# Performance work log

Measured on AMD Instinct MI355X. Metric: run time of the kernel, lower is better.

The kernel has to match this reference:

```python
import jax, jax.numpy as jnp
import numpy as np

N_NODES = 100000
N_EDGES = 800000


def gcn_layer(x, W, b, src, dst, n):
    # PyG GCNConv (normalize=True): x @ W, add self-loops, sym-normalized mean aggregation, + bias
    h = x @ W  # [N, out]
    deg = jax.ops.segment_sum(jnp.ones_like(src, dtype=h.dtype), dst, num_segments=n)
    dinv = jnp.where(deg > 0, jax.lax.rsqrt(jnp.maximum(deg, 1.0)), 0.0)
    norm = dinv[src] * dinv[dst]  # [E+N]
    msg = h[src] * norm[:, None]  # gather + scale
    out = jax.ops.segment_sum(msg, dst, num_segments=n)  # scatter-add
    return out + b


def setup_inputs() -> dict:
    key = jax.random.key(0)
    k1, k2, k3, k4 = jax.random.split(key, 4)
    x = jax.random.normal(k1, (N_NODES, 128), dtype=jnp.float32)
    edge_index = jax.random.randint(k2, (2, N_EDGES), 0, N_NODES, dtype=jnp.int64)
    W1 = jax.random.normal(k3, (128, 64), dtype=jnp.float32) * (1.0 / np.sqrt(128))
    b1 = jnp.zeros((64,), dtype=jnp.float32)
    W2 = jax.random.normal(k4, (64, 40), dtype=jnp.float32) * (1.0 / np.sqrt(64))
    b2 = jnp.zeros((40,), dtype=jnp.float32)
    return {"x": x, "edge_index": edge_index, "W1": W1, "b1": b1, "W2": W2, "b2": b2}


def reference(x, edge_index, W1, b1, W2, b2):
    n = x.shape[0]
    loop = jnp.arange(n, dtype=edge_index.dtype)
    src = jnp.concatenate([edge_index[0], loop])  # add self-loops
    dst = jnp.concatenate([edge_index[1], loop])
    h = jax.nn.relu(gcn_layer(x, W1, b1, src, dst, n))
    # dropout is identity in eval mode (self.training=False)
    out = gcn_layer(h, W2, b2, src, dst, n)
    return jax.nn.log_softmax(out, axis=1)
```

## Files before the change

kernel.cpp:

```cpp
#include <hip/hip_runtime.h>
#include <hip/hip_fp16.h>
#include <math.h>


typedef _Float16 f16x4 __attribute__((ext_vector_type(4)));
typedef _Float16 f16x8 __attribute__((ext_vector_type(8)));
typedef float    f32x4 __attribute__((ext_vector_type(4)));

__global__ void zero_kernel(int* __restrict__ p, int n) {
    int i = blockIdx.x * blockDim.x + threadIdx.x;
    if (i < n) p[i] = 0;
}

__global__ void deg_rank_kernel(const int* __restrict__ dst, int* __restrict__ degi,
                                int* __restrict__ rank, int E) {
    int i = blockIdx.x * blockDim.x + threadIdx.x;
    if (i < E) rank[i] = atomicAdd(&degi[dst[i]], 1);
}

__global__ __launch_bounds__(256) void blocksum_kernel(const int* __restrict__ degi,
                                                       int* __restrict__ partial, int n) {
    __shared__ int sm[256];
    int t = threadIdx.x;
    int base = blockIdx.x * 1024 + t * 4;
    int s = 0;
#pragma unroll
    for (int j = 0; j < 4; ++j) { int i = base + j; if (i < n) s += degi[i]; }
    sm[t] = s;
    __syncthreads();
    for (int off = 128; off > 0; off >>= 1) {
        if (t < off) sm[t] += sm[t + off];
        __syncthreads();
    }
    if (t == 0) partial[blockIdx.x] = sm[0];
}

__global__ __launch_bounds__(256) void offsets_kernel(int* __restrict__ degi,
                                                      const int* __restrict__ partial,
                                                      int* __restrict__ rowstart,
                                                      int n, int nb) {
    __shared__ int sm[256];
    __shared__ int pbase_s;
    int t = threadIdx.x;
    int pv = (t < nb) ? partial[t] : 0;
    sm[t] = pv;
    __syncthreads();
    for (int off = 1; off < 256; off <<= 1) {
        int x = (t >= off) ? sm[t - off] : 0;
        __syncthreads();
        sm[t] += x;
        __syncthreads();
    }
    if (t == 0) pbase_s = (blockIdx.x > 0) ? sm[blockIdx.x - 1] : 0;
    __syncthreads();
    int pbase = pbase_s;
    __syncthreads();

    int base = blockIdx.x * 1024 + t * 4;
    int v[4]; int s = 0;
#pragma unroll
    for (int j = 0; j < 4; ++j) { v[j] = (base + j < n) ? degi[base + j] : 0; s += v[j]; }
    sm[t] = s;
    __syncthreads();
    for (int off = 1; off < 256; off <<= 1) {
        int x = (t >= off) ? sm[t - off] : 0;
        __syncthreads();
        sm[t] += x;
        __syncthreads();
    }
    int run = pbase + (sm[t] - s);
#pragma unroll
    for (int j = 0; j < 4; ++j) {
        if (base + j < n) {
            rowstart[base + j] = run; run += v[j];
            ((float*)degi)[base + j] = rsqrtf((float)v[j] + 1.0f);
        }
    }
}

__global__ void fill_kernel(const int* __restrict__ src, const int* __restrict__ dst,
                            const int* __restrict__ rank, const float* __restrict__ dinv,
                            const int* __restrict__ rowstart, int2* __restrict__ csr, int E) {
    int e = blockIdx.x * blockDim.x + threadIdx.x;
    if (e >= E) return;
    int s = src[e], t = dst[e];
    float nrm = dinv[s] * dinv[t];
    unsigned short us = __half_as_ushort(__float2half_rn(nrm));
    int packed = (int)(((unsigned)us << 16) | us);
    int pos = rowstart[t] + rank[e];
    csr[pos] = make_int2(s, packed);
}

__global__ __launch_bounds__(256) void gemm1_mfma(const float* __restrict__ X,
                                                  const float* __restrict__ W,
                                                  _Float16* __restrict__ H, int n) {
    __shared__ _Float16 Xs[64 * 128];
    __shared__ _Float16 Ws[64 * 128];
    int t = threadIdx.x;
    int rowbase = blockIdx.x * 64;

    for (int i = t; i < 2048; i += 256) {
        int row = i >> 5;
        int k = (i & 31) * 4;
        int gr = rowbase + row; if (gr >= n) gr = n - 1;
        float4 v = *reinterpret_cast<const float4*>(X + (size_t)gr * 128 + k);
        f16x4 hv = { (_Float16)v.x, (_Float16)v.y, (_Float16)v.z, (_Float16)v.w };
        int idx = row * 128 + (k ^ ((row & 7) << 3));
        *reinterpret_cast<f16x4*>(&Xs[idx]) = hv;
    }
    for (int i = t; i < 2048; i += 256) {
        int k = i >> 4;
        int nn0 = (i & 15) * 4;
        float4 v = *reinterpret_cast<const float4*>(W + (size_t)k * 64 + nn0);
        const float* vp = reinterpret_cast<const float*>(&v);
#pragma unroll
        for (int j = 0; j < 4; ++j) {
            int nn = nn0 + j;
            Ws[nn * 128 + (k ^ ((nn & 7) << 3))] = (_Float16)vp[j];
        }
    }
    __syncthreads();

    int w = t >> 6;
    int l = t & 63;
    int lr = l & 15;
    int lk = l >> 4;
    int arow = 16 * w + lr;

    f16x8 a[4];
#pragma unroll
    for (int kc = 0; kc < 4; ++kc) {
        int k8 = kc * 32 + lk * 8;
        a[kc] = *reinterpret_cast<f16x8*>(&Xs[arow * 128 + (k8 ^ ((arow & 7) << 3))]);
    }
    f32x4 acc[4] = {};
#pragma unroll
    for (int nt = 0; nt < 4; ++nt) {
        int nrow = 16 * nt + lr;
#pragma unroll
        for (int kc = 0; kc < 4; ++kc) {
            int k8 = kc * 32 + lk * 8;
            f16x8 b = *reinterpret_cast<f16x8*>(&Ws[nrow * 128 + (k8 ^ ((nrow & 7) << 3))]);
            acc[nt] = __builtin_amdgcn_mfma_f32_16x16x32_f16(a[kc], b, acc[nt], 0, 0, 0);
        }
    }
#pragma unroll
    for (int nt = 0; nt < 4; ++nt) {
#pragma unroll
        for (int r = 0; r < 4; ++r) {
            int grow = rowbase + 16 * w + lk * 4 + r;
            if (grow < n) H[(size_t)grow * 64 + nt * 16 + lr] = (_Float16)acc[nt][r];
        }
    }
}

static __device__ __forceinline__ __half2 relu_h2(__half2 v) {
    unsigned u = *reinterpret_cast<unsigned*>(&v);
    unsigned neg = (u >> 15) & 0x00010001u;
    u &= ~(neg * 0xFFFFu);
    return *reinterpret_cast<__half2*>(&u);
}

template <bool RELU, bool BIAS>
__global__ __launch_bounds__(256) void gather64h_kernel(const __half* __restrict__ Hh,
                                                        const int2* __restrict__ csr,
                                                        const int* __restrict__ rowstart,
                                                        const float* __restrict__ dinv,
                                                        const float* __restrict__ b,
                                                        __half* __restrict__ Oh, int n, int E) {
    int gt = blockIdx.x * blockDim.x + threadIdx.x;
    int node = gt >> 3;
    if (node >= n) return;
    int fl = gt & 7;
    const float4* H4 = reinterpret_cast<const float4*>(Hh);
    int rs = rowstart[node];
    int re = (node + 1 < n) ? rowstart[node + 1] : E;
    __half2 acc[4];
#pragma unroll
    for (int q = 0; q < 4; ++q) acc[q] = __float2half2_rn(0.0f);

    int e = rs;
    while (__any(e < re)) {
        int srcrow[4]; __half2 nh[4]; float4 raw[4];
#pragma unroll
        for (int u = 0; u < 4; ++u) {
            int ee = e + u;
            bool valid = ee < re;
            int2 c = csr[valid ? ee : rs];
            srcrow[u] = valid ? c.x : 0;
            int ni = valid ? c.y : 0;
            nh[u] = *reinterpret_cast<__half2*>(&ni);
        }
#pragma unroll
        for (int u = 0; u < 4; ++u)
            raw[u] = H4[srcrow[u] * 8 + fl];
#pragma unroll
        for (int u = 0; u < 4; ++u) {
            const __half2* hp = reinterpret_cast<const __half2*>(&raw[u]);
#pragma unroll
            for (int q = 0; q < 4; ++q)
                acc[q] = __hfma2(hp[q], nh[u], acc[q]);
        }
        e += 4;
    }
    {
        float di = dinv[node];
        __half2 d2 = __float2half2_rn(di * di);
        float4 raw = H4[node * 8 + fl];
        const __half2* hp = reinterpret_cast<const __half2*>(&raw);
#pragma unroll
        for (int q = 0; q < 4; ++q) acc[q] = __hfma2(hp[q], d2, acc[q]);
    }
    if (BIAS) {
        float4 b0 = reinterpret_cast<const float4*>(b)[fl * 2];
        float4 b1 = reinterpret_cast<const float4*>(b)[fl * 2 + 1];
        acc[0] = __hadd2(acc[0], __float22half2_rn(make_float2(b0.x, b0.y)));
        acc[1] = __hadd2(acc[1], __float22half2_rn(make_float2(b0.z, b0.w)));
        acc[2] = __hadd2(acc[2], __float22half2_rn(make_float2(b1.x, b1.y)));
        acc[3] = __hadd2(acc[3], __float22half2_rn(make_float2(b1.z, b1.w)));
    }
    if (RELU) {
#pragma unroll
        for (int q = 0; q < 4; ++q) acc[q] = relu_h2(acc[q]);
    }
    float4 o;
    __half2* op = reinterpret_cast<__half2*>(&o);
#pragma unroll
    for (int q = 0; q < 4; ++q) op[q] = acc[q];
    *reinterpret_cast<float4*>(Oh + (size_t)node * 64 + fl * 8) = o;
}

__global__ __launch_bounds__(256) void gemm2_softmax_kernel(const __half* __restrict__ Xh,
                                                            const float* __restrict__ W,
                                                            const float* __restrict__ b,
                                                            float* __restrict__ out, int n) {
    constexpr int BM = 96, K = 64, C = 40, XP = 68, HP = 41;
    __shared__ float Xs[BM * XP];
    __shared__ float Ws[K * C];
    __shared__ float bs[C];
    __shared__ float rowm[BM], rowls[BM];
    int t = threadIdx.x;
    int tx = t % (C / 4);
    int ty = t / (C / 4);
    bool active = ty < BM / 4;
    int rowbase = blockIdx.x * BM;

    for (int i = t; i < K * C / 4; i += 256)
        ((float4*)Ws)[i] = ((const float4*)W)[i];
    if (t < C) bs[t] = b[t];
    for (int fi = t; fi < BM * 8; fi += 256) {
        int row = fi >> 3, kq = fi & 7;
        int gr = rowbase + row; if (gr >= n) gr = n - 1;
        float4 raw = reinterpret_cast<const float4*>(Xh + (size_t)gr * K)[kq];
        const __half2* hp = reinterpret_cast<const __half2*>(&raw);
        float2 f0 = __half22float2(hp[0]), f1 = __half22float2(hp[1]);
        float2 f2 = __half22float2(hp[2]), f3 = __half22float2(hp[3]);
        float* dp = &Xs[row * XP + kq * 8];
        *reinterpret_cast<float4*>(dp)     = make_float4(f0.x, f0.y, f1.x, f1.y);
        *reinterpret_cast<float4*>(dp + 4) = make_float4(f2.x, f2.y, f3.x, f3.y);
    }
    __syncthreads();

    float acc[4][4] = {};
    if (active) {
#pragma unroll
        for (int k0 = 0; k0 < K; k0 += 4) {
            float4 xq[4], wq[4];
#pragma unroll
            for (int i = 0; i < 4; ++i)
                xq[i] = *reinterpret_cast<const float4*>(&Xs[(ty * 4 + i) * XP + k0]);
#pragma unroll
            for (int j = 0; j < 4; ++j)
                wq[j] = *reinterpret_cast<const float4*>(&Ws[(k0 + j) * C + tx * 4]);
#pragma unroll
            for (int i = 0; i < 4; ++i) {
                const float* xa = reinterpret_cast<const float*>(&xq[i]);
#pragma unroll
                for (int j = 0; j < 4; ++j) {
                    const float* wb = reinterpret_cast<const float*>(&wq[j]);
                    acc[i][0] += xa[j] * wb[0];
                    acc[i][1] += xa[j] * wb[1];
                    acc[i][2] += xa[j] * wb[2];
                    acc[i][3] += xa[j] * wb[3];
                }
            }
        }
    }
    __syncthreads();
    float* Hs = Xs;
    if (active) {
#pragma unroll
        for (int i = 0; i < 4; ++i) {
            int r = ty * 4 + i;
#pragma unroll
            for (int j = 0; j < 4; ++j)
                Hs[r * HP + tx * 4 + j] = acc[i][j] + bs[tx * 4 + j];
        }
    }
    __syncthreads();
    if (t < BM) {
        float m = -INFINITY;
        for (int j = 0; j < C; ++j) m = fmaxf(m, Hs[t * HP + j]);
        float s = 0.f;
        for (int j = 0; j < C; ++j) s += __expf(Hs[t * HP + j] - m);
        rowm[t] = m; rowls[t] = __logf(s);
    }
    __syncthreads();
    for (int idx = t; idx < BM * C; idx += 256) {
        int r = idx / C, c = idx - r * C;
        int gr = rowbase + r;
        if (gr < n) out[(size_t)gr * C + c] = Hs[r * HP + c] - rowm[r] - rowls[r];
    }
}

extern "C" void kernel_launch(void* const* d_in, const int* in_sizes, int n_in,
                              void* d_out, int out_size, void* d_ws, size_t ws_size,
                              hipStream_t stream) {
    const float* x  = (const float*)d_in[0];
    const int*   ei = (const int*)d_in[1];
    const float* W1 = (const float*)d_in[2];
    const float* b1 = (const float*)d_in[3];
    const float* W2 = (const float*)d_in[4];
    const float* b2 = (const float*)d_in[5];
    float* out = (float*)d_out;

    const int n = in_sizes[0] / 128;
    const int E = in_sizes[1] / 2;
    const int* src = ei;
    const int* dst = ei + E;

    auto al = [](size_t x) { return (x + 255) & ~(size_t)255; };
    float* ws = (float*)d_ws;
    size_t o_deg  = 0;
    size_t o_cnt  = al(n);
    size_t o_part = o_cnt + al(n);
    size_t o_rank = o_part + 1024;
    size_t o_csr  = o_rank + al(E);
    size_t o_h1   = o_csr + al((size_t)2 * E);
    size_t o_out1 = o_h1 + al((size_t)n * 32);

    int*    degi     = (int*)(ws + o_deg);
    float*  dinv     = (float*)(ws + o_deg);
    int*    rowstart = (int*)(ws + o_cnt);
    int*    partial  = (int*)(ws + o_part);
    int*    rank     = (int*)(ws + o_rank);
    int2*   csr      = (int2*)(ws + o_csr);
    __half* h1       = (__half*)(ws + o_h1);
    __half* out1     = (__half*)(ws + o_out1);
    __half* agg2     = (__half*)(ws + o_h1);

    const int NB = (n + 1023) / 1024;

    zero_kernel<<<(n + 255) / 256, 256, 0, stream>>>(degi, n);
    deg_rank_kernel<<<(E + 255) / 256, 256, 0, stream>>>(dst, degi, rank, E);
    blocksum_kernel<<<NB, 256, 0, stream>>>(degi, partial, n);
    offsets_kernel<<<NB, 256, 0, stream>>>(degi, partial, rowstart, n, NB);
    fill_kernel<<<(E + 255) / 256, 256, 0, stream>>>(src, dst, rank, dinv, rowstart, csr, E);

    gemm1_mfma<<<(n + 63) / 64, 256, 0, stream>>>(x, W1, (_Float16*)h1, n);
    gather64h_kernel<true, true><<<((size_t)n * 8 + 255) / 256, 256, 0, stream>>>(
        h1, csr, rowstart, dinv, b1, out1, n, E);
    gather64h_kernel<false, false><<<((size_t)n * 8 + 255) / 256, 256, 0, stream>>>(
        out1, csr, rowstart, dinv, nullptr, agg2, n, E);
    gemm2_softmax_kernel<<<(n + 95) / 96, 256, 0, stream>>>(agg2, W2, b2, out, n);
}
```

Baseline: 144.2 us.

## Fuse layer-2 gather into GEMM2+softmax and load X directly into MFMA registers

The second-layer neighbor aggregation now runs inside the GEMM2/log-softmax kernel. Each block gathers 64 rows into shared memory and then applies W2 and the softmax, so the fp16 agg2 intermediate is never written to or read back from global memory, and one launch is removed. GEMM1 also stops staging X through LDS: each lane loads its fp32 A fragment straight from global memory and converts it to fp16 in registers. The cost is a smaller row tile per block (64 instead of 96), so W2 is reloaded by more blocks, and the gather's irregular latency now sits in front of the GEMM inside one block.

```diff
diff --git a/kernel.cpp b/kernel.cpp
--- a/kernel.cpp
+++ b/kernel.cpp
@@ -3,7 +3,6 @@
 #include <math.h>
 
 
-typedef _Float16 f16x4 __attribute__((ext_vector_type(4)));
 typedef _Float16 f16x8 __attribute__((ext_vector_type(8)));
 typedef float    f32x4 __attribute__((ext_vector_type(4)));
 
@@ -94,20 +93,10 @@
 __global__ __launch_bounds__(256) void gemm1_mfma(const float* __restrict__ X,
                                                   const float* __restrict__ W,
                                                   _Float16* __restrict__ H, int n) {
-    __shared__ _Float16 Xs[64 * 128];
     __shared__ _Float16 Ws[64 * 128];
     int t = threadIdx.x;
     int rowbase = blockIdx.x * 64;
 
-    for (int i = t; i < 2048; i += 256) {
-        int row = i >> 5;
-        int k = (i & 31) * 4;
-        int gr = rowbase + row; if (gr >= n) gr = n - 1;
-        float4 v = *reinterpret_cast<const float4*>(X + (size_t)gr * 128 + k);
-        f16x4 hv = { (_Float16)v.x, (_Float16)v.y, (_Float16)v.z, (_Float16)v.w };
-        int idx = row * 128 + (k ^ ((row & 7) << 3));
-        *reinterpret_cast<f16x4*>(&Xs[idx]) = hv;
-    }
     for (int i = t; i < 2048; i += 256) {
         int k = i >> 4;
         int nn0 = (i & 15) * 4;
@@ -119,20 +108,26 @@
             Ws[nn * 128 + (k ^ ((nn & 7) << 3))] = (_Float16)vp[j];
         }
     }
-    __syncthreads();
 
     int w = t >> 6;
     int l = t & 63;
     int lr = l & 15;
     int lk = l >> 4;
-    int arow = 16 * w + lr;
+    int arow = rowbase + 16 * w + lr;
+    int ar = arow < n ? arow : n - 1;
 
     f16x8 a[4];
 #pragma unroll
     for (int kc = 0; kc < 4; ++kc) {
-        int k8 = kc * 32 + lk * 8;
-        a[kc] = *reinterpret_cast<f16x8*>(&Xs[arow * 128 + (k8 ^ ((arow & 7) << 3))]);
-    }
+        const float* xp = X + (size_t)ar * 128 + kc * 32 + lk * 8;
+        float4 v0 = *reinterpret_cast<const float4*>(xp);
+        float4 v1 = *reinterpret_cast<const float4*>(xp + 4);
+        f16x8 hv = { (_Float16)v0.x, (_Float16)v0.y, (_Float16)v0.z, (_Float16)v0.w,
+                     (_Float16)v1.x, (_Float16)v1.y, (_Float16)v1.z, (_Float16)v1.w };
+        a[kc] = hv;
+    }
+    __syncthreads();
+
     f32x4 acc[4] = {};
 #pragma unroll
     for (int nt = 0; nt < 4; ++nt) {
@@ -230,37 +225,77 @@
     *reinterpret_cast<float4*>(Oh + (size_t)node * 64 + fl * 8) = o;
 }
 
-__global__ __launch_bounds__(256) void gemm2_softmax_kernel(const __half* __restrict__ Xh,
-                                                            const float* __restrict__ W,
-                                                            const float* __restrict__ b,
-                                                            float* __restrict__ out, int n) {
-    constexpr int BM = 96, K = 64, C = 40, XP = 68, HP = 41;
+__global__ __launch_bounds__(256) void gather_gemm2_softmax(
+        const __half* __restrict__ Hh, const int2* __restrict__ csr,
+        const int* __restrict__ rowstart, const float* __restrict__ dinv,
+        const float* __restrict__ W, const float* __restrict__ b,
+        float* __restrict__ out, int n, int E) {
+    constexpr int BM = 64, K = 64, C = 40, XP = 68, HP = 41;
     __shared__ float Xs[BM * XP];
     __shared__ float Ws[K * C];
     __shared__ float bs[C];
     __shared__ float rowm[BM], rowls[BM];
     int t = threadIdx.x;
+    int rowbase = blockIdx.x * BM;
+
+    for (int i = t; i < K * C / 4; i += 256)
+        ((float4*)Ws)[i] = ((const float4*)W)[i];
+    if (t < C) bs[t] = b[t];
+
+    int team = t >> 3, fl = t & 7;
+    const float4* H4 = reinterpret_cast<const float4*>(Hh);
+#pragma unroll
+    for (int pass = 0; pass < 2; ++pass) {
+        int lrow = team + pass * 32;
+        int node = rowbase + lrow;
+        __half2 acc[4];
+#pragma unroll
+        for (int q = 0; q < 4; ++q) acc[q] = __float2half2_rn(0.0f);
+        if (node < n) {
+            int rs = rowstart[node];
+            int re = (node + 1 < n) ? rowstart[node + 1] : E;
+            int e = rs;
+            while (__any(e < re)) {
+                int srcrow[4]; __half2 nh[4]; float4 raw[4];
+#pragma unroll
+                for (int u = 0; u < 4; ++u) {
+                    int ee = e + u;
+                    bool valid = ee < re;
+                    int2 c = csr[valid ? ee : rs];
+                    srcrow[u] = valid ? c.x : 0;
+                    int ni = valid ? c.y : 0;
+                    nh[u] = *reinterpret_cast<__half2*>(&ni);
+                }
+#pragma unroll
+                for (int u = 0; u < 4; ++u)
+                    raw[u] = H4[srcrow[u] * 8 + fl];
+#pragma unroll
+                for (int u = 0; u < 4; ++u) {
+                    const __half2* hp = reinterpret_cast<const __half2*>(&raw[u]);
+#pragma unroll
+                    for (int q = 0; q < 4; ++q)
+                        acc[q] = __hfma2(hp[q], nh[u], acc[q]);
+                }
+                e += 4;
+            }
+            float di = dinv[node];
+            __half2 d2 = __float2half2_rn(di * di);
+            float4 raw = H4[node * 8 + fl];
+            const __half2* hp = reinterpret_cast<const __half2*>(&raw);
+#pragma unroll
+            for (int q = 0; q < 4; ++q) acc[q] = __hfma2(hp[q], d2, acc[q]);
+        }
+        float* dp = &Xs[lrow * XP + fl * 8];
+        float2 f0 = __half22float2(acc[0]), f1 = __half22float2(acc[1]);
+        float2 f2 = __half22float2(acc[2]), f3 = __half22float2(acc[3]);
+        *reinterpret_cast<float4*>(dp)     = make_float4(f0.x, f0.y, f1.x, f1.y);
+        *reinterpret_cast<float4*>(dp + 4) = make_float4(f2.x, f2.y, f3.x, f3.y);
+    }
+    __syncthreads();
+
     int tx = t % (C / 4);
     int ty = t / (C / 4);
     bool active = ty < BM / 4;
-    int rowbase = blockIdx.x * BM;
-
-    for (int i = t; i < K * C / 4; i += 256)
-        ((float4*)Ws)[i] = ((const float4*)W)[i];
-    if (t < C) bs[t] = b[t];
-    for (int fi = t; fi < BM * 8; fi += 256) {
-        int row = fi >> 3, kq = fi & 7;
-        int gr = rowbase + row; if (gr >= n) gr = n - 1;
-        float4 raw = reinterpret_cast<const float4*>(Xh + (size_t)gr * K)[kq];
-        const __half2* hp = reinterpret_cast<const __half2*>(&raw);
-        float2 f0 = __half22float2(hp[0]), f1 = __half22float2(hp[1]);
-        float2 f2 = __half22float2(hp[2]), f3 = __half22float2(hp[3]);
-        float* dp = &Xs[row * XP + kq * 8];
-        *reinterpret_cast<float4*>(dp)     = make_float4(f0.x, f0.y, f1.x, f1.y);
-        *reinterpret_cast<float4*>(dp + 4) = make_float4(f2.x, f2.y, f3.x, f3.y);
-    }
-    __syncthreads();
-
     float acc[4][4] = {};
     if (active) {
 #pragma unroll
@@ -347,7 +382,6 @@
     int2*   csr      = (int2*)(ws + o_csr);
     __half* h1       = (__half*)(ws + o_h1);
     __half* out1     = (__half*)(ws + o_out1);
-    __half* agg2     = (__half*)(ws + o_h1);
 
     const int NB = (n + 1023) / 1024;
 
@@ -360,7 +394,6 @@
     gemm1_mfma<<<(n + 63) / 64, 256, 0, stream>>>(x, W1, (_Float16*)h1, n);
     gather64h_kernel<true, true><<<((size_t)n * 8 + 255) / 256, 256, 0, stream>>>(
         h1, csr, rowstart, dinv, b1, out1, n, E);
-    gather64h_kernel<false, false><<<((size_t)n * 8 + 255) / 256, 256, 0, stream>>>(
-        out1, csr, rowstart, dinv, nullptr, agg2, n, E);
-    gemm2_softmax_kernel<<<(n + 95) / 96, 256, 0, stream>>>(agg2, W2, b2, out, n);
-}
+    gather_gemm2_softmax<<<(n + 63) / 64, 256, 0, stream>>>(
+        out1, csr, rowstart, dinv, W2, b2, out, n, E);
+}
```

After: 137.4 us. -4.7%, faster.
